# Kernel tuning notes

Measured on AMD Instinct MI355X. Metric: run time of the kernel, lower is better.

Reference implementation:

```python
import jax, jax.numpy as jnp
import numpy as np

N = 8192
E = 262144
D_IN = 128
D_OUT = 128

def setup_inputs() -> dict:
    key = jax.random.key(0)
    k1, k2, k3, k4 = jax.random.split(key, 4)
    x = jax.random.normal(k1, (N, D_IN), dtype=jnp.float32)
    edge_index = jax.random.randint(k2, (2, E), 0, N, dtype=jnp.int64)
    W = jax.random.normal(k3, (D_OUT, D_IN), dtype=jnp.float32) * 0.05
    b = jax.random.normal(k4, (D_OUT,), dtype=jnp.float32) * 0.05
    return {"x": x, "edge_index": edge_index, "W": W, "b": b}

def reference(x, edge_index, W, b):
    num_nodes = x.shape[0]
    # Dense adjacency: adj[src, dst] = 1.0 (duplicate edges set, not add)
    adj = jnp.zeros((num_nodes, num_nodes), dtype=x.dtype)
    adj = adj.at[edge_index[0], edge_index[1]].set(1.0)
    adj = adj + jnp.eye(num_nodes, dtype=x.dtype)  # self-loops (added on top)
    degree = adj.sum(axis=1, keepdims=True)
    degree = jnp.where(degree > 0, degree, jnp.ones_like(degree))
    adj = adj / degree  # row-normalize
    out = adj @ x               # [N, D_IN] aggregation
    out = out @ W.T + b         # nn.Linear
    return out
```

## Files before the change

kernel.cpp:

```cpp
#include <hip/hip_runtime.h>


typedef unsigned int uint32;

#define NNODES 8192
#define DF 128
#define DF4 (DF / 4)
#define WPR 256
#define CAP 128

#define BM_BYTES  ((size_t)NNODES * WPR * 4)
#define ZROW_OFF  BM_BYTES
#define ZERO_BYTES (BM_BYTES + 1024)

__device__ __forceinline__ float4 f4add(float4 a, float4 b) {
    return make_float4(a.x + b.x, a.y + b.y, a.z + b.z, a.w + b.w);
}

__global__ __launch_bounds__(256) void scatter_dedup(
    const int* __restrict__ ei, int E, uint32* __restrict__ bm)
{
    int e = blockIdx.x * 256 + threadIdx.x;
    if (e >= E) return;
    int src = ei[e];
    int dst = ei[E + e];
    atomicOr(&bm[(size_t)src * WPR + (dst >> 5)], 1u << (dst & 31));
}

__global__ __launch_bounds__(256, 4) void gcn_fused(
    const float* __restrict__ x, const float* __restrict__ W,
    const float* __restrict__ b, const uint32* __restrict__ bm,
    const float4* __restrict__ zrow, float* __restrict__ out)
{
    __shared__ int   nbr[4][CAP];
    __shared__ __align__(16) float agg[4][DF];

    const int t    = threadIdx.x;
    const int w    = t >> 6;
    const int lane = t & 63;
    const int node0 = blockIdx.x * 4;
    const int node  = node0 + w;

    const uint32* r = bm + (size_t)node * WPR;
    const uint4 ww = ((const uint4*)r)[lane];
    int cpop = __popc(ww.x) + __popc(ww.y) + __popc(ww.z) + __popc(ww.w);
    int v = cpop;
    #pragma unroll
    for (int d = 1; d < 64; d <<= 1) {
        int up = __shfl_up(v, d);
        if (lane >= d) v += up;
    }
    int off = v - cpop;
    const int total = __shfl(v, 63);
    {
        uint32 arr[4] = {ww.x, ww.y, ww.z, ww.w};
        #pragma unroll
        for (int q = 0; q < 4; ++q) {
            uint32 word = arr[q];
            int base = (4 * lane + q) << 5;
            while (word) {
                int bit = __ffs(word) - 1; word &= word - 1;
                if (off < CAP) nbr[w][off] = base + bit;
                off++;
            }
        }
    }
    const int cm = min(total, CAP);
    const int L  = (cm + 15) & ~15;
    for (int k = cm + lane; k < L; k += 64) nbr[w][k] = -1;
    __syncthreads();

    const int s = lane >> 5, c = lane & 31;
    const float4* x4 = (const float4*)x;
    float4 acc = make_float4(0.f, 0.f, 0.f, 0.f);

    if (total <= CAP) {
        for (int k = s; k < L; k += 16) {
            int j0 = nbr[w][k],      j1 = nbr[w][k + 2],
                j2 = nbr[w][k + 4],  j3 = nbr[w][k + 6],
                j4 = nbr[w][k + 8],  j5 = nbr[w][k + 10],
                j6 = nbr[w][k + 12], j7 = nbr[w][k + 14];
            const float4* p0 = (j0 >= 0) ? x4 + (size_t)j0 * DF4 + c : zrow + c;
            const float4* p1 = (j1 >= 0) ? x4 + (size_t)j1 * DF4 + c : zrow + c;
            const float4* p2 = (j2 >= 0) ? x4 + (size_t)j2 * DF4 + c : zrow + c;
            const float4* p3 = (j3 >= 0) ? x4 + (size_t)j3 * DF4 + c : zrow + c;
            const float4* p4 = (j4 >= 0) ? x4 + (size_t)j4 * DF4 + c : zrow + c;
            const float4* p5 = (j5 >= 0) ? x4 + (size_t)j5 * DF4 + c : zrow + c;
            const float4* p6 = (j6 >= 0) ? x4 + (size_t)j6 * DF4 + c : zrow + c;
            const float4* p7 = (j7 >= 0) ? x4 + (size_t)j7 * DF4 + c : zrow + c;
            float4 v0 = *p0, v1 = *p1, v2 = *p2, v3 = *p3;
            float4 v4 = *p4, v5 = *p5, v6 = *p6, v7 = *p7;
            acc = f4add(acc, f4add(f4add(v0, v1), f4add(v2, v3)));
            acc = f4add(acc, f4add(f4add(v4, v5), f4add(v6, v7)));
        }
        acc.x += __shfl_down(acc.x, 32);
        acc.y += __shfl_down(acc.y, 32);
        acc.z += __shfl_down(acc.z, 32);
        acc.w += __shfl_down(acc.w, 32);
    } else if (lane < 32) {
        for (int wd = 0; wd < WPR; ++wd) {
            uint32 word = r[wd];
            int base = wd << 5;
            while (word) {
                int bit = __ffs(word) - 1; word &= word - 1;
                acc = f4add(acc, x4[(size_t)(base + bit) * DF4 + c]);
            }
        }
    }

    if (lane < 32) {
        float4 self = x4[(size_t)node * DF4 + c];
        float inv = 1.0f / (float)(total + 1);
        float4 a = f4add(acc, self);
        *(float4*)&agg[w][c * 4] =
            make_float4(a.x * inv, a.y * inv, a.z * inv, a.w * inv);
    }
    __syncthreads();

    {
        const int d = t & 127, h = t >> 7;
        const float4* Wrow = (const float4*)(W + (size_t)d * DF);
        float bias = b[d];
        float s0 = bias, s1 = bias;
        #pragma unroll 8
        for (int c4 = 0; c4 < DF4; ++c4) {
            float4 wv = Wrow[c4];
            float4 g0 = *(const float4*)&agg[2 * h + 0][c4 * 4];
            float4 g1 = *(const float4*)&agg[2 * h + 1][c4 * 4];
            s0 += wv.x * g0.x + wv.y * g0.y + wv.z * g0.z + wv.w * g0.w;
            s1 += wv.x * g1.x + wv.y * g1.y + wv.z * g1.z + wv.w * g1.w;
        }
        out[(size_t)(node0 + 2 * h + 0) * DF + d] = s0;
        out[(size_t)(node0 + 2 * h + 1) * DF + d] = s1;
    }
}

extern "C" void kernel_launch(void* const* d_in, const int* in_sizes, int n_in,
                              void* d_out, int out_size, void* d_ws, size_t ws_size,
                              hipStream_t stream) {
    const float* x = (const float*)d_in[0];
    const int*  ei = (const int*)d_in[1];
    const float* W = (const float*)d_in[2];
    const float* b = (const float*)d_in[3];
    float* out = (float*)d_out;

    uint32* bm   = (uint32*)d_ws;
    float4* zrow = (float4*)((char*)d_ws + ZROW_OFF);
    const int E = in_sizes[1] / 2;

    hipMemsetAsync(d_ws, 0, ZERO_BYTES, stream);

    scatter_dedup<<<dim3((E + 255) / 256), dim3(256), 0, stream>>>(ei, E, bm);
    gcn_fused<<<dim3(NNODES / 4), dim3(256), 0, stream>>>(
        x, W, b, bm, zrow, out);
}
```

Measured before the change: 112.7 us.

## Apply linear transform before neighbor aggregation using separate node GEMM kernel

Reorders the computation to z = x·Wᵀ first and then aggregates rows of z, instead of aggregating x and multiplying each block's four rows by W. This is valid because row normalization is linear. A transposed copy of W is built by extra blocks in the scatter kernel, and a new tiled GEMM kernel computes z once per node with shared-memory reuse of x rows. The gather kernel then only sums z rows, scales by the inverse degree and adds the bias, which removes the per-block full-W reads and the second barrier. In exchange it adds a kernel launch and a round trip of z through global memory.

```diff
diff --git a/kernel.cpp b/kernel.cpp
--- a/kernel.cpp
+++ b/kernel.cpp
@@ -11,35 +11,83 @@
 
 #define BM_BYTES  ((size_t)NNODES * WPR * 4)
 #define ZROW_OFF  BM_BYTES
+#define WT_OFF    (ZROW_OFF + 1024)
+#define Z_OFF     (WT_OFF + (size_t)DF * DF * 4)
 #define ZERO_BYTES (BM_BYTES + 1024)
 
 __device__ __forceinline__ float4 f4add(float4 a, float4 b) {
     return make_float4(a.x + b.x, a.y + b.y, a.z + b.z, a.w + b.w);
 }
 
-__global__ __launch_bounds__(256) void scatter_dedup(
-    const int* __restrict__ ei, int E, uint32* __restrict__ bm)
+__global__ __launch_bounds__(256) void scatter_wt(
+    const int* __restrict__ ei, int E, const float* __restrict__ W,
+    uint32* __restrict__ bm, float* __restrict__ Wt)
 {
-    int e = blockIdx.x * 256 + threadIdx.x;
-    if (e >= E) return;
-    int src = ei[e];
-    int dst = ei[E + e];
-    atomicOr(&bm[(size_t)src * WPR + (dst >> 5)], 1u << (dst & 31));
+    const int blk = blockIdx.x, t = threadIdx.x;
+    const int nsb = (E + 255) >> 8;
+    if (blk < nsb) {
+        int e = blk * 256 + t;
+        if (e < E) {
+            int src = ei[e];
+            int dst = ei[E + e];
+            atomicOr(&bm[(size_t)src * WPR + (dst >> 5)], 1u << (dst & 31));
+        }
+    } else {
+        for (int i = (blk - nsb) * 256 + t; i < DF * DF; i += 16 * 256) {
+            int k = i >> 7, d = i & (DF - 1);
+            Wt[i] = W[d * DF + k];
+        }
+    }
 }
 
-__global__ __launch_bounds__(256, 4) void gcn_fused(
-    const float* __restrict__ x, const float* __restrict__ W,
-    const float* __restrict__ b, const uint32* __restrict__ bm,
-    const float4* __restrict__ zrow, float* __restrict__ out)
+__global__ __launch_bounds__(256) void node_gemm(
+    const float* __restrict__ x, const float* __restrict__ Wt,
+    float* __restrict__ z)
 {
-    __shared__ int   nbr[4][CAP];
-    __shared__ __align__(16) float agg[4][DF];
+    __shared__ float xs[32][DF];
+    const int t = threadIdx.x;
+    const int n0 = blockIdx.x * 32;
+
+    const float4* x4 = (const float4*)x + (size_t)n0 * DF4;
+    float4* xs4 = (float4*)xs;
+    for (int i = t; i < 32 * DF4; i += 256) xs4[i] = x4[i];
+    __syncthreads();
+
+    const int c = t & 31;
+    const int ng = t >> 5;
+    const float4* Wt4 = (const float4*)Wt;
+
+    float4 a0 = make_float4(0, 0, 0, 0), a1 = a0, a2 = a0, a3 = a0;
+    #pragma unroll 4
+    for (int k = 0; k < DF; ++k) {
+        float4 wv = Wt4[k * DF4 + c];
+        float x0 = xs[4 * ng + 0][k];
+        float x1 = xs[4 * ng + 1][k];
+        float x2 = xs[4 * ng + 2][k];
+        float x3 = xs[4 * ng + 3][k];
+        a0.x += x0 * wv.x; a0.y += x0 * wv.y; a0.z += x0 * wv.z; a0.w += x0 * wv.w;
+        a1.x += x1 * wv.x; a1.y += x1 * wv.y; a1.z += x1 * wv.z; a1.w += x1 * wv.w;
+        a2.x += x2 * wv.x; a2.y += x2 * wv.y; a2.z += x2 * wv.z; a2.w += x2 * wv.w;
+        a3.x += x3 * wv.x; a3.y += x3 * wv.y; a3.z += x3 * wv.z; a3.w += x3 * wv.w;
+    }
+    float4* z4 = (float4*)z;
+    z4[(size_t)(n0 + 4 * ng + 0) * DF4 + c] = a0;
+    z4[(size_t)(n0 + 4 * ng + 1) * DF4 + c] = a1;
+    z4[(size_t)(n0 + 4 * ng + 2) * DF4 + c] = a2;
+    z4[(size_t)(n0 + 4 * ng + 3) * DF4 + c] = a3;
+}
+
+__global__ __launch_bounds__(256) void gather_z(
+    const float4* __restrict__ z4, const uint32* __restrict__ bm,
+    const float4* __restrict__ zrow, const float* __restrict__ b,
+    float* __restrict__ out)
+{
+    __shared__ int nbr[4][CAP];
 
     const int t    = threadIdx.x;
     const int w    = t >> 6;
     const int lane = t & 63;
-    const int node0 = blockIdx.x * 4;
-    const int node  = node0 + w;
+    const int node = blockIdx.x * 4 + w;
 
     const uint32* r = bm + (size_t)node * WPR;
     const uint4 ww = ((const uint4*)r)[lane];
@@ -68,10 +116,8 @@
     const int cm = min(total, CAP);
     const int L  = (cm + 15) & ~15;
     for (int k = cm + lane; k < L; k += 64) nbr[w][k] = -1;
-    __syncthreads();
 
     const int s = lane >> 5, c = lane & 31;
-    const float4* x4 = (const float4*)x;
     float4 acc = make_float4(0.f, 0.f, 0.f, 0.f);
 
     if (total <= CAP) {
@@ -80,14 +126,14 @@
                 j2 = nbr[w][k + 4],  j3 = nbr[w][k + 6],
                 j4 = nbr[w][k + 8],  j5 = nbr[w][k + 10],
                 j6 = nbr[w][k + 12], j7 = nbr[w][k + 14];
-            const float4* p0 = (j0 >= 0) ? x4 + (size_t)j0 * DF4 + c : zrow + c;
-            const float4* p1 = (j1 >= 0) ? x4 + (size_t)j1 * DF4 + c : zrow + c;
-            const float4* p2 = (j2 >= 0) ? x4 + (size_t)j2 * DF4 + c : zrow + c;
-            const float4* p3 = (j3 >= 0) ? x4 + (size_t)j3 * DF4 + c : zrow + c;
-            const float4* p4 = (j4 >= 0) ? x4 + (size_t)j4 * DF4 + c : zrow + c;
-            const float4* p5 = (j5 >= 0) ? x4 + (size_t)j5 * DF4 + c : zrow + c;
-            const float4* p6 = (j6 >= 0) ? x4 + (size_t)j6 * DF4 + c : zrow + c;
-            const float4* p7 = (j7 >= 0) ? x4 + (size_t)j7 * DF4 + c : zrow + c;
+            const float4* p0 = (j0 >= 0) ? z4 + (size_t)j0 * DF4 + c : zrow + c;
+            const float4* p1 = (j1 >= 0) ? z4 + (size_t)j1 * DF4 + c : zrow + c;
+            const float4* p2 = (j2 >= 0) ? z4 + (size_t)j2 * DF4 + c : zrow + c;
+            const float4* p3 = (j3 >= 0) ? z4 + (size_t)j3 * DF4 + c : zrow + c;
+            const float4* p4 = (j4 >= 0) ? z4 + (size_t)j4 * DF4 + c : zrow + c;
+            const float4* p5 = (j5 >= 0) ? z4 + (size_t)j5 * DF4 + c : zrow + c;
+            const float4* p6 = (j6 >= 0) ? z4 + (size_t)j6 * DF4 + c : zrow + c;
+            const float4* p7 = (j7 >= 0) ? z4 + (size_t)j7 * DF4 + c : zrow + c;
             float4 v0 = *p0, v1 = *p1, v2 = *p2, v3 = *p3;
             float4 v4 = *p4, v5 = *p5, v6 = *p6, v7 = *p7;
             acc = f4add(acc, f4add(f4add(v0, v1), f4add(v2, v3)));
@@ -103,35 +149,19 @@
             int base = wd << 5;
             while (word) {
                 int bit = __ffs(word) - 1; word &= word - 1;
-                acc = f4add(acc, x4[(size_t)(base + bit) * DF4 + c]);
+                acc = f4add(acc, z4[(size_t)(base + bit) * DF4 + c]);
             }
         }
     }
 
     if (lane < 32) {
-        float4 self = x4[(size_t)node * DF4 + c];
+        float4 self = z4[(size_t)node * DF4 + c];
+        float4 bb = ((const float4*)b)[c];
         float inv = 1.0f / (float)(total + 1);
         float4 a = f4add(acc, self);
-        *(float4*)&agg[w][c * 4] =
-            make_float4(a.x * inv, a.y * inv, a.z * inv, a.w * inv);
-    }
-    __syncthreads();
-
-    {
-        const int d = t & 127, h = t >> 7;
-        const float4* Wrow = (const float4*)(W + (size_t)d * DF);
-        float bias = b[d];
-        float s0 = bias, s1 = bias;
-        #pragma unroll 8
-        for (int c4 = 0; c4 < DF4; ++c4) {
-            float4 wv = Wrow[c4];
-            float4 g0 = *(const float4*)&agg[2 * h + 0][c4 * 4];
-            float4 g1 = *(const float4*)&agg[2 * h + 1][c4 * 4];
-            s0 += wv.x * g0.x + wv.y * g0.y + wv.z * g0.z + wv.w * g0.w;
-            s1 += wv.x * g1.x + wv.y * g1.y + wv.z * g1.z + wv.w * g1.w;
-        }
-        out[(size_t)(node0 + 2 * h + 0) * DF + d] = s0;
-        out[(size_t)(node0 + 2 * h + 1) * DF + d] = s1;
+        ((float4*)out)[(size_t)node * DF4 + c] =
+            make_float4(a.x * inv + bb.x, a.y * inv + bb.y,
+                        a.z * inv + bb.z, a.w * inv + bb.w);
     }
 }
 
@@ -144,13 +174,19 @@
     const float* b = (const float*)d_in[3];
     float* out = (float*)d_out;
 
-    uint32* bm   = (uint32*)d_ws;
-    float4* zrow = (float4*)((char*)d_ws + ZROW_OFF);
+    char* ws = (char*)d_ws;
+    uint32* bm   = (uint32*)ws;
+    float4* zrow = (float4*)(ws + ZROW_OFF);
+    float*  Wt   = (float*)(ws + WT_OFF);
+    float*  z    = (float*)(ws + Z_OFF);
+
     const int E = in_sizes[1] / 2;
+    const int nsb = (E + 255) / 256;
 
     hipMemsetAsync(d_ws, 0, ZERO_BYTES, stream);
 
-    scatter_dedup<<<dim3((E + 255) / 256), dim3(256), 0, stream>>>(ei, E, bm);
-    gcn_fused<<<dim3(NNODES / 4), dim3(256), 0, stream>>>(
-        x, W, b, bm, zrow, out);
+    scatter_wt<<<dim3(nsb + 16), dim3(256), 0, stream>>>(ei, E, W, bm, Wt);
+    node_gemm<<<dim3(NNODES / 32), dim3(256), 0, stream>>>(x, Wt, z);
+    gather_z<<<dim3(NNODES / 4), dim3(256), 0, stream>>>(
+        (const float4*)z, bm, zrow, b, out);
 }
```

Result: faster. 100.7 us (-10.6%).
